# Performance work log

Hardware: AMD Instinct MI355X
Metric: run time of the kernel (lower is better)

Reference implementation:

```python
import jax, jax.numpy as jnp
import numpy as np


def setup_inputs() -> dict:
    key = jax.random.key(0)
    k1, k2, k3 = jax.random.split(key, 3)
    B, T, C, H, W = 4, 1024, 64, 8, 8
    E = C * H * W  # 4096 == embed_dim
    x = jax.random.normal(k1, (B, T, C, H, W), dtype=jnp.float32)
    Wqkv = jax.random.normal(k2, (E, 3 * E), dtype=jnp.float32) * (E ** -0.5)
    Wout = jax.random.normal(k3, (E, E), dtype=jnp.float32) * (E ** -0.5)
    bout = jnp.zeros((E,), dtype=jnp.float32)
    return {"x": x, "Wqkv": Wqkv, "Wout": Wout, "bout": bout}


def reference(x, Wqkv, Wout, bout):
    B, T, C, H, W = x.shape
    E = C * H * W
    heads = 8
    dh = E // heads
    # NOTE: original scales by embed_dim**-0.5, NOT head_dim**-0.5
    scale = E ** -0.5

    xf = x.reshape(B, T, E)                      # [B,T,E]
    qkv = xf @ Wqkv                              # [B,T,3E]
    q, k, v = jnp.split(qkv, 3, axis=-1)
    q = q.reshape(B, T, heads, dh)
    k = k.reshape(B, T, heads, dh)
    v = v.reshape(B, T, heads, dh)

    scores = jnp.einsum('bthd,bshd->bhts', q, k) * scale  # [B,h,T,T]
    attn = jax.nn.softmax(scores, axis=-1)
    out = jnp.einsum('bhts,bshd->bthd', attn, v)           # [B,T,h,dh]
    out = out.reshape(B, T, E) @ Wout + bout               # [B,T,E]
    return out.reshape(B, T, C, H, W)
```

## Files before the change

kernel.cpp:

```cpp
#include <hip/hip_runtime.h>
#include <hip/hip_bf16.h>

typedef __attribute__((ext_vector_type(8))) __bf16 bf16x8;
typedef __attribute__((ext_vector_type(4))) __bf16 bf16x4;
typedef __attribute__((ext_vector_type(4))) float f32x4;
typedef __attribute__((ext_vector_type(4))) int i32x4;

#define MFMA16(a, b, c) __builtin_amdgcn_mfma_f32_16x16x32_bf16((a), (b), (c), 0, 0, 0)
#define MFMAI8(a, b, c) __builtin_amdgcn_mfma_i32_16x16x64_i8((a), (b), (c), 0, 0, 0)

__global__ __launch_bounds__(256) void k_prep(const float* __restrict__ x,
                                              __bf16* __restrict__ xb,
                                              char* __restrict__ xi8,
                                              float* __restrict__ sa,
                                              const float* __restrict__ Wqkv,
                                              __bf16* __restrict__ wT) {
  __shared__ float tl[64][68];
  int id = blockIdx.x, tid = threadIdx.x;
  if (id < 4096) {
    int row = id;
    const float* src = x + (size_t)row * 4096 + tid * 16;
    float arr[16];
#pragma unroll
    for (int j = 0; j < 4; ++j) {
      float4 v = ((const float4*)src)[j];
      arr[j * 4 + 0] = v.x; arr[j * 4 + 1] = v.y;
      arr[j * 4 + 2] = v.z; arr[j * 4 + 3] = v.w;
    }
    float m = 0.f;
#pragma unroll
    for (int e = 0; e < 16; ++e) m = fmaxf(m, fabsf(arr[e]));
#pragma unroll
    for (int off = 32; off; off >>= 1) m = fmaxf(m, __shfl_xor(m, off, 64));
    float* wmx = &tl[0][0];
    if ((tid & 63) == 0) wmx[tid >> 6] = m;
    __syncthreads();
    m = fmaxf(fmaxf(wmx[0], wmx[1]), fmaxf(wmx[2], wmx[3]));
    m = fmaxf(m, 1e-20f);
    float inv = 127.f / m;
    __bf16* db = xb + (size_t)row * 4096 + tid * 16;
#pragma unroll
    for (int j = 0; j < 2; ++j) {
      bf16x8 o;
#pragma unroll
      for (int e = 0; e < 8; ++e) o[e] = (__bf16)arr[j * 8 + e];
      *(bf16x8*)(db + j * 8) = o;
    }
    int pk[4];
#pragma unroll
    for (int j = 0; j < 4; ++j) {
      int wv = 0;
#pragma unroll
      for (int e = 0; e < 4; ++e) {
        int q = (int)__builtin_rintf(arr[j * 4 + e] * inv);
        q = q < -127 ? -127 : (q > 127 ? 127 : q);
        wv |= (q & 255) << (e * 8);
      }
      pk[j] = wv;
    }
    int4 pv; pv.x = pk[0]; pv.y = pk[1]; pv.z = pk[2]; pv.w = pk[3];
    *(int4*)(xi8 + (size_t)row * 4096 + tid * 16) = pv;
    if (tid == 0) sa[row] = m / 127.f;
    return;
  }
  int t = id - 4096;
  int c0 = (t % 192) * 64, r0 = (t / 192) * 64;
  const int R = 4096, C = 12288;
#pragma unroll
  for (int j = 0; j < 4; ++j) {
    int idx = j * 256 + tid;
    int row = idx >> 4, q4 = (idx & 15) * 4;
    float4 v = *(const float4*)(Wqkv + (size_t)(r0 + row) * C + c0 + q4);
    tl[row][q4 + 0] = v.x; tl[row][q4 + 1] = v.y;
    tl[row][q4 + 2] = v.z; tl[row][q4 + 3] = v.w;
  }
  __syncthreads();
#pragma unroll
  for (int j = 0; j < 2; ++j) {
    int idx = j * 256 + tid;
    int orow = idx >> 3, ch = (idx & 7) * 8;
    bf16x8 pk;
#pragma unroll
    for (int e = 0; e < 8; ++e) pk[e] = (__bf16)tl[ch + e][orow];
    *(bf16x8*)(wT + (size_t)(c0 + orow) * R + r0 + ch) = pk;
  }
}

__global__ __launch_bounds__(256) void k_quantW(const __bf16* __restrict__ wT,
                                                char* __restrict__ wi8,
                                                float* __restrict__ sb) {
  int row = blockIdx.x, tid = threadIdx.x;
  const __bf16* src = wT + (size_t)row * 4096 + tid * 16;
  float arr[16];
#pragma unroll
  for (int j = 0; j < 2; ++j) {
    bf16x8 v = *(const bf16x8*)(src + j * 8);
#pragma unroll
    for (int e = 0; e < 8; ++e) arr[j * 8 + e] = (float)v[e];
  }
  float m = 0.f;
#pragma unroll
  for (int e = 0; e < 16; ++e) m = fmaxf(m, fabsf(arr[e]));
#pragma unroll
  for (int off = 32; off; off >>= 1) m = fmaxf(m, __shfl_xor(m, off, 64));
  __shared__ float wmx[4];
  if ((tid & 63) == 0) wmx[tid >> 6] = m;
  __syncthreads();
  m = fmaxf(fmaxf(wmx[0], wmx[1]), fmaxf(wmx[2], wmx[3]));
  m = fmaxf(m, 1e-20f);
  float inv = 127.f / m;
  int pk[4];
#pragma unroll
  for (int j = 0; j < 4; ++j) {
    int w = 0;
#pragma unroll
    for (int e = 0; e < 4; ++e) {
      int q = (int)__builtin_rintf(arr[j * 4 + e] * inv);
      q = q < -127 ? -127 : (q > 127 ? 127 : q);
      w |= (q & 255) << (e * 8);
    }
    pk[j] = w;
  }
  int4 pv; pv.x = pk[0]; pv.y = pk[1]; pv.z = pk[2]; pv.w = pk[3];
  *(int4*)(wi8 + (size_t)row * 4096 + tid * 16) = pv;
  if (tid == 0) sb[row] = m / 127.f;
}

__global__ __launch_bounds__(256) void k_post1(const __bf16* __restrict__ qkv,
                                               __bf16* __restrict__ vt,
                                               const float* __restrict__ Wout,
                                               __bf16* __restrict__ woT) {
  __shared__ float tlf[64][68];
  __shared__ __bf16 tlh[64][72];
  int id = blockIdx.x, tid = threadIdx.x;
  if (id < 4096) {
    int bx = id & 7, by = (id >> 3) & 15, p = id >> 7;
    int b = p >> 3, h = p & 7;
    int d0 = bx * 64, s0 = by * 64;
    const __bf16* src = qkv + (size_t)b * 1024 * 12288 + 8192 + h * 512;
#pragma unroll
    for (int j = 0; j < 2; ++j) {
      int idx = j * 256 + tid;
      int row = idx >> 3, ch = (idx & 7) * 8;
      bf16x8 v = *(const bf16x8*)(src + (size_t)(s0 + row) * 12288 + d0 + ch);
#pragma unroll
      for (int e = 0; e < 8; ++e) tlh[row][ch + e] = v[e];
    }
    __syncthreads();
#pragma unroll
    for (int j = 0; j < 2; ++j) {
      int idx = j * 256 + tid;
      int orow = idx >> 3, ch = (idx & 7) * 8;
      bf16x8 pk;
#pragma unroll
      for (int e = 0; e < 8; ++e) pk[e] = tlh[ch + e][orow];
      *(bf16x8*)(vt + (size_t)p * 524288 + (size_t)(d0 + orow) * 1024 + s0 + ch) = pk;
    }
    return;
  }
  int t = id - 4096;
  int c0 = (t & 63) * 64, r0 = (t >> 6) * 64;
  const int R = 4096, C = 4096;
#pragma unroll
  for (int j = 0; j < 4; ++j) {
    int idx = j * 256 + tid;
    int row = idx >> 4, q4 = (idx & 15) * 4;
    float4 v = *(const float4*)(Wout + (size_t)(r0 + row) * C + c0 + q4);
    tlf[row][q4 + 0] = v.x; tlf[row][q4 + 1] = v.y;
    tlf[row][q4 + 2] = v.z; tlf[row][q4 + 3] = v.w;
  }
  __syncthreads();
#pragma unroll
  for (int j = 0; j < 2; ++j) {
    int idx = j * 256 + tid;
    int orow = idx >> 3, ch = (idx & 7) * 8;
    bf16x8 pk;
#pragma unroll
    for (int e = 0; e < 8; ++e) pk[e] = (__bf16)tlf[ch + e][orow];
    *(bf16x8*)(woT + (size_t)(c0 + orow) * R + r0 + ch) = pk;
  }
}

#define BARRIER() __builtin_amdgcn_s_barrier()
#define SCHED0() __builtin_amdgcn_sched_barrier(0)
#define VMC8() asm volatile("s_waitcnt vmcnt(8)" ::: "memory")
#define LGKM(N)                                                   \
  do {                                                            \
    asm volatile("s_waitcnt lgkmcnt(" #N ")" ::: "memory");       \
    __builtin_amdgcn_sched_barrier(0);                            \
  } while (0)

#define LDA(AF, buf, mh)                                                      \
  do {                                                                        \
    _Pragma("unroll") for (int mi = 0; mi < 4; ++mi) {                        \
      int r = wm * 64 + mi * 16 + r16;                                        \
      _Pragma("unroll") for (int ks = 0; ks < 2; ++ks) {                      \
        int gg = ks * 4 + g;                                                  \
        AF[mi][ks] = *(const bf16x8*)(ldsB + (buf)*32768 + (mh)*16384 +       \
                                      r * 128 + ((gg ^ (r & 7)) << 4));       \
      }                                                                       \
    }                                                                         \
  } while (0)

#define LDB(BQ, buf, nh)                                                      \
  do {                                                                        \
    _Pragma("unroll") for (int ni = 0; ni < 2; ++ni) {                        \
      int r = wn * 32 + ni * 16 + r16;                                        \
      _Pragma("unroll") for (int ks = 0; ks < 2; ++ks) {                      \
        int gg = ks * 4 + g;                                                  \
        BQ[ni][ks] = *(const bf16x8*)(ldsB + 65536 + (buf)*32768 +            \
                                      (nh)*16384 + r * 128 +                  \
                                      ((gg ^ (r & 7)) << 4));                 \
      }                                                                       \
    }                                                                         \
  } while (0)

#define QUAD(AF, mh, nh, BQ)                                                  \
  do {                                                                        \
    __builtin_amdgcn_s_setprio(1);                                            \
    _Pragma("unroll") for (int ks = 0; ks < 2; ++ks)                          \
        _Pragma("unroll") for (int mi = 0; mi < 4; ++mi)                      \
            _Pragma("unroll") for (int ni = 0; ni < 2; ++ni)                  \
                acc[(mh)*4 + mi][(nh)*2 + ni] =                               \
                    MFMA16(AF[mi][ks], BQ[ni][ks],                            \
                           acc[(mh)*4 + mi][(nh)*2 + ni]);                    \
    __builtin_amdgcn_s_setprio(0);                                            \
    __builtin_amdgcn_sched_barrier(0);                                        \
  } while (0)

#define STAGE_A(mh, tau)                                                      \
  do {                                                                        \
    int tc = (tau) < NT ? (tau) : NT - 1;                                     \
    char* dbase = ldsB + ((tau)&1) * 32768 + (mh)*16384;                      \
    _Pragma("unroll") for (int i = 0; i < 2; ++i)                             \
        __builtin_amdgcn_global_load_lds(                                     \
            (const __attribute__((address_space(1))) void*)(Ap +              \
                offA[i][mh] + tc * 64),                                       \
            (__attribute__((address_space(3))) void*)(dbase +                 \
                (i * 512 + w * 64) * 16), 16, 0, 0);                          \
  } while (0)

#define STAGE_B(nh, tau)                                                      \
  do {                                                                        \
    int tc = (tau) < NT ? (tau) : NT - 1;                                     \
    char* dbase = ldsB + 65536 + ((tau)&1) * 32768 + (nh)*16384;              \
    _Pragma("unroll") for (int i = 0; i < 2; ++i)                             \
        __builtin_amdgcn_global_load_lds(                                     \
            (const __attribute__((address_space(1))) void*)(Bp +              \
                offB[i][nh] + tc * 64),                                       \
            (__attribute__((address_space(3))) void*)(dbase +                 \
                (i * 512 + w * 64) * 16), 16, 0, 0);                          \
  } while (0)

#define STAGE4(tau)                                                           \
  do {                                                                        \
    STAGE_A(0, tau); STAGE_B(0, tau); STAGE_B(1, tau); STAGE_A(1, tau);       \
  } while (0)

#define TILE_LOOP()                                                           \
  STAGE4(0);                                                                  \
  STAGE4(1);                                                                  \
  for (int t = 0; t < NT; ++t) {                                              \
    int buf = t & 1;                                                          \
    VMC8();                                                                   \
    BARRIER();                                                                \
    LDA(af, buf, 0);                                                          \
    LDB(bq0, buf, 0);                                                         \
    SCHED0();                                                                 \
    LDB(bq1, buf, 1);                                                         \
    SCHED0();                                                                 \
    LDA(af2, buf, 1);                                                         \
    LGKM(12);                                                                 \
    QUAD(af, 0, 0, bq0);                                                      \
    LGKM(8);                                                                  \
    QUAD(af, 0, 1, bq1);                                                      \
    LGKM(0);                                                                  \
    BARRIER();                                                                \
    STAGE4(t + 2);                                                            \
    QUAD(af2, 1, 1, bq1);                                                     \
    QUAD(af2, 1, 0, bq0);                                                     \
  }

#define SETUP_OFFSETS()                                                       \
  int offA[2][2], offB[2][2];                                                 \
  _Pragma("unroll") for (int i = 0; i < 2; ++i) {                             \
    int c = i * 512 + tid;                                                    \
    int r = c >> 3, slot = c & 7;                                             \
    int colsw = (slot ^ (r & 7)) << 3;                                        \
    _Pragma("unroll") for (int h = 0; h < 2; ++h) {                           \
      int RA = (r >> 6) * 128 + h * 64 + (r & 63);                            \
      int RB = (r >> 5) * 64 + h * 32 + (r & 31);                             \
      offA[i][h] = RA * lda + colsw;                                          \
      offB[i][h] = RB * ldb + colsw;                                          \
    }                                                                         \
  }

template <int MODE>
__global__ __launch_bounds__(512, 2) void k_gemm8(
    const __bf16* __restrict__ Abase, const __bf16* __restrict__ Bbase,
    void* __restrict__ Cout, const float* __restrict__ aux,
    int lda, int ldb, int N, int K) {
  __shared__ __align__(128) __bf16 lds[65536];
  char* ldsB = (char*)lds;
  int tid = threadIdx.x;
  int w = tid >> 6, lane = tid & 63;
  int r16 = lane & 15, g = lane >> 4;
  int wm = w >> 2, wn = w & 3;

  int bx, by, z = blockIdx.z;
  if (MODE <= 1) {
    int gx = gridDim.x, gy = gridDim.y;
    int RX = gx >> 2, RY = gy >> 1;
    int orig = blockIdx.y * gx + blockIdx.x;
    int xcd = orig & 7, idx = orig >> 3;
    int lbx = idx / RY, lby = idx - lbx * RY;
    bx = (xcd & 3) * RX + lbx;
    by = (xcd >> 2) * RY + lby;
  } else if (MODE == 2) {
    int i = blockIdx.z * 16 + blockIdx.y * 4 + blockIdx.x;
    z = (i & 7) | (((i >> 7) & 3) << 3);
    int qt = (i >> 3) & 15;
    by = qt >> 2; bx = qt & 3;
  } else {
    int i = blockIdx.z * 8 + blockIdx.y * 2 + blockIdx.x;
    z = (i & 7) | (((i >> 6) & 3) << 3);
    int qt = (i >> 3) & 7;
    by = qt >> 1; bx = qt & 1;
  }
  int m0 = by * 256, n0 = bx * 256;

  const __bf16 *Ap, *Bp;
  if (MODE == 2) {
    int b = z >> 3, h = z & 7;
    Ap = Abase + (size_t)b * 1024 * 12288 + h * 512;
    Bp = Abase + (size_t)b * 1024 * 12288 + 4096 + h * 512;
  } else if (MODE == 3) {
    Ap = Abase + (size_t)z * 1048576;
    Bp = Bbase + (size_t)z * 524288;
  } else {
    Ap = Abase; Bp = Bbase;
  }
  Ap += (size_t)m0 * lda;
  Bp += (size_t)n0 * ldb;
  SETUP_OFFSETS()

  int NT = K >> 6;
  f32x4 acc[8][4];
#pragma unroll
  for (int a = 0; a < 8; ++a)
#pragma unroll
    for (int bq = 0; bq < 4; ++bq) acc[a][bq] = f32x4{0.f, 0.f, 0.f, 0.f};
  bf16x8 af[4][2], af2[4][2], bq0[2][2], bq1[2][2];

  TILE_LOOP()

  if (MODE == 2) {
    asm volatile("s_waitcnt vmcnt(0)" ::: "memory");
    __syncthreads();
    float* Lbuf = (float*)ldsB;
#pragma unroll
    for (int mig = 0; mig < 8; ++mig) {
#pragma unroll
      for (int ii = 0; ii < 4; ++ii) {
        int row = m0 + wm * 128 + mig * 16 + g * 4 + ii;
        float s = 0.f;
#pragma unroll
        for (int nig = 0; nig < 4; ++nig) {
          int col = n0 + wn * 64 + nig * 16 + r16;
          float e = __expf(acc[mig][nig][ii] * 0.015625f);
          ((__bf16*)Cout)[(size_t)z * 1048576 + (size_t)row * 1024 + col] =
              (__bf16)e;
          s += e;
        }
        s += __shfl_xor(s, 1, 64);
        s += __shfl_xor(s, 2, 64);
        s += __shfl_xor(s, 4, 64);
        s += __shfl_xor(s, 8, 64);
        if (r16 == 0)
          Lbuf[(wm * 4 + wn) * 128 + mig * 16 + g * 4 + ii] = s;
      }
    }
    __syncthreads();
    if (tid < 256) {
      int wmi = tid >> 7, rl = tid & 127;
      const float* base = Lbuf + wmi * 512;
      float s = base[rl] + base[128 + rl] + base[256 + rl] + base[384 + rl];
      ((float*)aux)[z * 4096 + bx * 1024 + m0 + tid] = s;
    }
    return;
  }

#pragma unroll
  for (int mig = 0; mig < 8; ++mig) {
#pragma unroll
    for (int ii = 0; ii < 4; ++ii) {
      int row = m0 + wm * 128 + mig * 16 + g * 4 + ii;
      float lval = 0.f;
      if (MODE == 3)
        lval = aux[z * 4096 + row] + aux[z * 4096 + 1024 + row] +
               aux[z * 4096 + 2048 + row] + aux[z * 4096 + 3072 + row];
#pragma unroll
      for (int nig = 0; nig < 4; ++nig) {
        int col = n0 + wn * 64 + nig * 16 + r16;
        float v = acc[mig][nig][ii];
        if (MODE == 0) {
          ((__bf16*)Cout)[(size_t)row * N + col] = (__bf16)v;
        } else if (MODE == 1) {
          ((float*)Cout)[(size_t)row * N + col] = v + aux[col];
        } else if (MODE == 3) {
          ((__bf16*)Cout)[(size_t)((z >> 3) * 1024 + row) * 4096 +
                          (z & 7) * 512 + col] = (__bf16)(v / lval);
        }
      }
    }
  }
}

#define I8_SWZ(r) (((r) & 3) ^ (((r) >> 2) & 3))

#define I8_STAGE(tau, base)                                                   \
  do {                                                                        \
    int tc = (tau) < NT ? (tau) : NT - 1;                                     \
    char* da = (base);                                                        \
    _Pragma("unroll") for (int h = 0; h < 2; ++h) {                           \
      __builtin_amdgcn_global_load_lds(                                       \
          (const __attribute__((address_space(1))) void*)(Ap + offA[h] +      \
                                                          tc * 64),           \
          (__attribute__((address_space(3))) void*)(da + h * 8192 +           \
              w * 1024), 16, 0, 0);                                           \
      __builtin_amdgcn_global_load_lds(                                       \
          (const __attribute__((address_space(1))) void*)(Bp + offB[h] +      \
                                                          tc * 64),           \
          (__attribute__((address_space(3))) void*)(da + 16384 + h * 8192 +   \
              w * 1024), 16, 0, 0);                                           \
    }                                                                         \
  } while (0)

#define I8_QUAD(MIBASE)                                                       \
  do {                                                                        \
    __builtin_amdgcn_s_setprio(1);                                            \
    _Pragma("unroll") for (int mi = 0; mi < 4; ++mi)                          \
        _Pragma("unroll") for (int ni = 0; ni < 4; ++ni)                      \
            acc[(MIBASE) + mi][ni] = MFMAI8(af[mi], bq[ni],                   \
                                            acc[(MIBASE) + mi][ni]);          \
    __builtin_amdgcn_s_setprio(0);                                            \
    __builtin_amdgcn_sched_barrier(0);                                        \
  } while (0)

__global__ __launch_bounds__(512, 2) void k_gemm_i8(
    const char* __restrict__ Abase, const char* __restrict__ Bbase,
    __bf16* __restrict__ Cout, const float* __restrict__ sa,
    const float* __restrict__ sb) {
  __shared__ __align__(128) char ldsB[98304];
  const int lda = 4096, ldb = 4096, NT = 64;
  int tid = threadIdx.x;
  int w = tid >> 6, lane = tid & 63;
  int r16 = lane & 15, g = lane >> 4;
  int wm = w >> 2, wn = w & 3;

  int gx = gridDim.x, gy = gridDim.y;
  int RX = gx >> 2, RY = gy >> 1;
  int orig = blockIdx.y * gx + blockIdx.x;
  int xcd = orig & 7, idx = orig >> 3;
  int lbx = idx / RY, lby = idx - lbx * RY;
  int bx = (xcd & 3) * RX + lbx;
  int by = (xcd >> 2) * RY + lby;
  int m0 = by * 256, n0 = bx * 256;

  const char* Ap = Abase + (size_t)m0 * lda;
  const char* Bp = Bbase + (size_t)n0 * ldb;

  int offA[2], offB[2];
  {
    int rl = tid >> 2, slot = tid & 3;
    int slotg = (slot ^ I8_SWZ(rl)) << 4;
#pragma unroll
    for (int h = 0; h < 2; ++h) {
      offA[h] = (h * 128 + rl) * lda + slotg;
      offB[h] = (h * 128 + rl) * ldb + slotg;
    }
  }

  i32x4 acc[8][4];
#pragma unroll
  for (int a = 0; a < 8; ++a)
#pragma unroll
    for (int b = 0; b < 4; ++b) acc[a][b] = i32x4{0, 0, 0, 0};
  i32x4 af[4], af2[4], bq[4];

  I8_STAGE(0, ldsB);
  I8_STAGE(1, ldsB + 32768);
  I8_STAGE(2, ldsB + 65536);
  int bufo = 0;
  for (int t = 0; t < NT; ++t) {
    char* base = ldsB + bufo * 32768;
    VMC8();
    BARRIER();
    {
      char* bbase = base + 16384 + (wn >> 1) * 8192;
#pragma unroll
      for (int ni = 0; ni < 4; ++ni) {
        int rb = (wn & 1) * 64 + ni * 16 + r16;
        bq[ni] = *(const i32x4*)(bbase + rb * 64 + ((g ^ I8_SWZ(rb)) << 4));
      }
    }
    SCHED0();
    {
      char* abase = base + wm * 8192;
#pragma unroll
      for (int mi = 0; mi < 4; ++mi) {
        int r = mi * 16 + r16;
        af[mi] = *(const i32x4*)(abase + r * 64 + ((g ^ I8_SWZ(r)) << 4));
      }
      SCHED0();
#pragma unroll
      for (int mi = 0; mi < 4; ++mi) {
        int r = 64 + mi * 16 + r16;
        af2[mi] = *(const i32x4*)(abase + r * 64 + ((g ^ I8_SWZ(r)) << 4));
      }
    }
    LGKM(4);
    I8_QUAD(0);
    LGKM(0);
    BARRIER();
    I8_STAGE(t + 3, base);
#pragma unroll
    for (int mi = 0; mi < 4; ++mi) af[mi] = af2[mi];
    I8_QUAD(4);
    bufo = (bufo == 2) ? 0 : bufo + 1;
  }

#pragma unroll
  for (int mig = 0; mig < 8; ++mig) {
#pragma unroll
    for (int ii = 0; ii < 4; ++ii) {
      int row = m0 + wm * 128 + ((mig >> 2) * 64) + (mig & 3) * 16 + g * 4 + ii;
      float sav = sa[row];
#pragma unroll
      for (int nig = 0; nig < 4; ++nig) {
        int col = n0 + wn * 64 + nig * 16 + r16;
        float v = (float)acc[mig][nig][ii] * sav * sb[col];
        Cout[(size_t)row * 12288 + col] = (__bf16)v;
      }
    }
  }
}

extern "C" void kernel_launch(void* const* d_in, const int* in_sizes, int n_in,
                              void* d_out, int out_size, void* d_ws, size_t ws_size,
                              hipStream_t stream) {
  const float* x = (const float*)d_in[0];
  const float* Wqkv = (const float*)d_in[1];
  const float* Wout = (const float*)d_in[2];
  const float* bout = (const float*)d_in[3];
  float* out = (float*)d_out;
  char* ws = (char*)d_ws;

  __bf16* xb = (__bf16*)(ws);
  __bf16* wT = (__bf16*)(ws + 33554432);
  __bf16* P = (__bf16*)(ws + 33554432);
  __bf16* woT = (__bf16*)(ws + 33554432 + 67108864);
  __bf16* qkv = (__bf16*)(ws + 134217728);
  char* wi8 = (char*)(ws + 234881024);
  __bf16* vt = (__bf16*)(ws + 234881024);

  char* xi8 = (char*)d_out;
  float* sa = (float*)((char*)d_out + 16777216);
  float* sb = (float*)((char*)d_out + 16777216 + 65536);
  float* Lpart = (float*)((char*)d_out + 33554432);

  k_prep<<<16384, 256, 0, stream>>>(x, xb, xi8, sa, Wqkv, wT);
  k_quantW<<<8192, 256, 0, stream>>>(wT, wi8, sb);
  k_gemm_i8<<<dim3(32, 16), 512, 0, stream>>>(xi8, wi8, qkv, sa, sb);
  k_gemm8<0><<<dim3(16, 16), 512, 0, stream>>>(
      xb, wT + (size_t)8192 * 4096, qkv + 8192, nullptr, 4096, 4096, 12288, 4096);
  k_post1<<<8192, 256, 0, stream>>>(qkv, vt, Wout, woT);
  k_gemm8<2><<<dim3(4, 4, 32), 512, 0, stream>>>(qkv, qkv, P, Lpart, 12288, 12288, 1024, 512);
  k_gemm8<3><<<dim3(2, 4, 32), 512, 0, stream>>>(P, vt, xb, Lpart, 1024, 1024, 512, 1024);
  k_gemm8<1><<<dim3(16, 16), 512, 0, stream>>>(xb, woT, out, bout, 4096, 4096, 4096, 4096);
}
```

Before: 580.5 us.

## Double K-tile depth in int8 GEMM with two-stage 128-byte LDS pipeline

Changes the int8 QKV GEMM from a three-buffer pipeline with 64-byte K tiles to a two-buffer pipeline with 128-byte K tiles. The loop trip count halves, a new XOR swizzle covers 8 slots per row, and the B fragments are split into halves so MFMAs can begin after partial LDS waits. The goal is fewer barriers and less loop overhead per unit of work. In exchange, LDS use rises to 128KB and register pressure goes up, which could lower occupancy under launch_bounds(512,2). Prefetch depth also drops from three stages to two.

```diff
diff --git a/kernel.cpp b/kernel.cpp
--- a/kernel.cpp
+++ b/kernel.cpp
@@ -416,43 +416,67 @@
   }
 }
 
-#define I8_SWZ(r) (((r) & 3) ^ (((r) >> 2) & 3))
-
-#define I8_STAGE(tau, base)                                                   \
+#define I8_LDA(AF, buf, mh)                                                   \
+  do {                                                                        \
+    _Pragma("unroll") for (int mi = 0; mi < 4; ++mi) {                        \
+      int r = wm * 128 + (mh)*64 + mi * 16 + r16;                             \
+      _Pragma("unroll") for (int ks = 0; ks < 2; ++ks) {                      \
+        int gg = ks * 4 + g;                                                  \
+        AF[mi][ks] = *(const i32x4*)(ldsB + (buf)*65536 + r * 128 +           \
+                                     ((gg ^ (r & 7)) << 4));                  \
+      }                                                                       \
+    }                                                                         \
+  } while (0)
+
+#define I8_LDB(BQ, buf, np)                                                   \
+  do {                                                                        \
+    _Pragma("unroll") for (int nj = 0; nj < 2; ++nj) {                        \
+      int r = wn * 64 + ((np)*2 + nj) * 16 + r16;                             \
+      _Pragma("unroll") for (int ks = 0; ks < 2; ++ks) {                      \
+        int gg = ks * 4 + g;                                                  \
+        BQ[nj][ks] = *(const i32x4*)(ldsB + 32768 + (buf)*65536 + r * 128 +   \
+                                     ((gg ^ (r & 7)) << 4));                  \
+      }                                                                       \
+    }                                                                         \
+  } while (0)
+
+#define I8_QUAD(AF, mh, np, BQ)                                               \
+  do {                                                                        \
+    __builtin_amdgcn_s_setprio(1);                                            \
+    _Pragma("unroll") for (int ks = 0; ks < 2; ++ks)                          \
+        _Pragma("unroll") for (int mi = 0; mi < 4; ++mi)                      \
+            _Pragma("unroll") for (int nj = 0; nj < 2; ++nj)                  \
+                acc[(mh)*4 + mi][(np)*2 + nj] =                               \
+                    MFMAI8(AF[mi][ks], BQ[nj][ks],                            \
+                           acc[(mh)*4 + mi][(np)*2 + nj]);                    \
+    __builtin_amdgcn_s_setprio(0);                                            \
+    __builtin_amdgcn_sched_barrier(0);                                        \
+  } while (0)
+
+#define I8_STAGE(tau)                                                         \
   do {                                                                        \
     int tc = (tau) < NT ? (tau) : NT - 1;                                     \
-    char* da = (base);                                                        \
-    _Pragma("unroll") for (int h = 0; h < 2; ++h) {                           \
+    char* da = ldsB + ((tau)&1) * 65536;                                      \
+    _Pragma("unroll") for (int i = 0; i < 4; ++i) {                           \
       __builtin_amdgcn_global_load_lds(                                       \
-          (const __attribute__((address_space(1))) void*)(Ap + offA[h] +      \
-                                                          tc * 64),           \
-          (__attribute__((address_space(3))) void*)(da + h * 8192 +           \
+          (const __attribute__((address_space(1))) void*)(Ap + offA[i] +      \
+                                                          tc * 128),          \
+          (__attribute__((address_space(3))) void*)(da + i * 8192 +           \
               w * 1024), 16, 0, 0);                                           \
       __builtin_amdgcn_global_load_lds(                                       \
-          (const __attribute__((address_space(1))) void*)(Bp + offB[h] +      \
-                                                          tc * 64),           \
-          (__attribute__((address_space(3))) void*)(da + 16384 + h * 8192 +   \
+          (const __attribute__((address_space(1))) void*)(Bp + offB[i] +      \
+                                                          tc * 128),          \
+          (__attribute__((address_space(3))) void*)(da + 32768 + i * 8192 +   \
               w * 1024), 16, 0, 0);                                           \
     }                                                                         \
-  } while (0)
-
-#define I8_QUAD(MIBASE)                                                       \
-  do {                                                                        \
-    __builtin_amdgcn_s_setprio(1);                                            \
-    _Pragma("unroll") for (int mi = 0; mi < 4; ++mi)                          \
-        _Pragma("unroll") for (int ni = 0; ni < 4; ++ni)                      \
-            acc[(MIBASE) + mi][ni] = MFMAI8(af[mi], bq[ni],                   \
-                                            acc[(MIBASE) + mi][ni]);          \
-    __builtin_amdgcn_s_setprio(0);                                            \
-    __builtin_amdgcn_sched_barrier(0);                                        \
   } while (0)
 
 __global__ __launch_bounds__(512, 2) void k_gemm_i8(
     const char* __restrict__ Abase, const char* __restrict__ Bbase,
     __bf16* __restrict__ Cout, const float* __restrict__ sa,
     const float* __restrict__ sb) {
-  __shared__ __align__(128) char ldsB[98304];
-  const int lda = 4096, ldb = 4096, NT = 64;
+  __shared__ __align__(128) char ldsB[131072];
+  const int lda = 4096, ldb = 4096, NT = 32;
   int tid = threadIdx.x;
   int w = tid >> 6, lane = tid & 63;
   int r16 = lane & 15, g = lane >> 4;
@@ -470,15 +494,14 @@
   const char* Ap = Abase + (size_t)m0 * lda;
   const char* Bp = Bbase + (size_t)n0 * ldb;
 
-  int offA[2], offB[2];
-  {
-    int rl = tid >> 2, slot = tid & 3;
-    int slotg = (slot ^ I8_SWZ(rl)) << 4;
-#pragma unroll
-    for (int h = 0; h < 2; ++h) {
-      offA[h] = (h * 128 + rl) * lda + slotg;
-      offB[h] = (h * 128 + rl) * ldb + slotg;
-    }
+  int offA[4], offB[4];
+#pragma unroll
+  for (int i = 0; i < 4; ++i) {
+    int c = i * 512 + tid;
+    int r = c >> 3, slot = c & 7;
+    int colsw = (slot ^ (r & 7)) << 4;
+    offA[i] = r * lda + colsw;
+    offB[i] = r * ldb + colsw;
   }
 
   i32x4 acc[8][4];
@@ -486,48 +509,29 @@
   for (int a = 0; a < 8; ++a)
 #pragma unroll
     for (int b = 0; b < 4; ++b) acc[a][b] = i32x4{0, 0, 0, 0};
-  i32x4 af[4], af2[4], bq[4];
-
-  I8_STAGE(0, ldsB);
-  I8_STAGE(1, ldsB + 32768);
-  I8_STAGE(2, ldsB + 65536);
-  int bufo = 0;
+  i32x4 af[4][2], af2[4][2], bq0[2][2], bq1[2][2];
+
+  I8_STAGE(0);
+  I8_STAGE(1);
   for (int t = 0; t < NT; ++t) {
-    char* base = ldsB + bufo * 32768;
+    int buf = t & 1;
     VMC8();
     BARRIER();
-    {
-      char* bbase = base + 16384 + (wn >> 1) * 8192;
-#pragma unroll
-      for (int ni = 0; ni < 4; ++ni) {
-        int rb = (wn & 1) * 64 + ni * 16 + r16;
-        bq[ni] = *(const i32x4*)(bbase + rb * 64 + ((g ^ I8_SWZ(rb)) << 4));
-      }
-    }
+    I8_LDA(af, buf, 0);
+    I8_LDB(bq0, buf, 0);
     SCHED0();
-    {
-      char* abase = base + wm * 8192;
-#pragma unroll
-      for (int mi = 0; mi < 4; ++mi) {
-        int r = mi * 16 + r16;
-        af[mi] = *(const i32x4*)(abase + r * 64 + ((g ^ I8_SWZ(r)) << 4));
-      }
-      SCHED0();
-#pragma unroll
-      for (int mi = 0; mi < 4; ++mi) {
-        int r = 64 + mi * 16 + r16;
-        af2[mi] = *(const i32x4*)(abase + r * 64 + ((g ^ I8_SWZ(r)) << 4));
-      }
-    }
-    LGKM(4);
-    I8_QUAD(0);
+    I8_LDB(bq1, buf, 1);
+    SCHED0();
+    I8_LDA(af2, buf, 1);
+    LGKM(12);
+    I8_QUAD(af, 0, 0, bq0);
+    LGKM(8);
+    I8_QUAD(af, 0, 1, bq1);
     LGKM(0);
     BARRIER();
-    I8_STAGE(t + 3, base);
-#pragma unroll
-    for (int mi = 0; mi < 4; ++mi) af[mi] = af2[mi];
-    I8_QUAD(4);
-    bufo = (bufo == 2) ? 0 : bufo + 1;
+    I8_STAGE(t + 2);
+    I8_QUAD(af2, 1, 1, bq1);
+    I8_QUAD(af2, 1, 0, bq0);
   }
 
 #pragma unroll
```

Result: faster. 565.3 us (-2.6%).
